# Optimization experiments

Hardware: AMD Instinct MI355X
Metric: run time of the kernel (lower is better)

Reference implementation:

```python
import jax, jax.numpy as jnp
import numpy as np
from jax import lax

A = -0.75  # torch bicubic cubic-kernel coefficient

def _cubic(t):
    t = jnp.abs(t)
    return jnp.where(t <= 1.0, ((A + 2.0) * t - (A + 3.0)) * t * t + 1.0,
                     jnp.where(t < 2.0, A * (((t - 5.0) * t + 8.0) * t - 4.0), 0.0))

def _up2_1d(x, axis):
    # torch F.interpolate(scale_factor=2, mode='bicubic', align_corners=False) along one axis
    n = x.shape[axis]
    src = (jnp.arange(2 * n, dtype=jnp.float32) + 0.5) / 2.0 - 0.5
    i0 = jnp.floor(src).astype(jnp.int32)
    taps = i0[:, None] + jnp.arange(-1, 3)          # [2n,4]
    w = _cubic(src[:, None] - taps.astype(jnp.float32))
    g = jnp.take(x, jnp.clip(taps, 0, n - 1), axis=axis)  # clamp = border replicate
    wshape = [1] * g.ndim
    wshape[axis] = 2 * n
    wshape[axis + 1] = 4
    return jnp.sum(g * w.reshape(wshape), axis=axis + 1)

def bicubic_x2(x):
    return _up2_1d(_up2_1d(x, 2), 3)

def conv2d(x, w, b, stride=1, pad=0):
    y = lax.conv_general_dilated(x, w, (stride, stride), [(pad, pad), (pad, pad)],
                                 dimension_numbers=('NCHW', 'OIHW', 'NCHW'))
    return y + b[None, :, None, None]

def lrelu(x):
    return jax.nn.leaky_relu(x, 0.2)

def resblock(x, w1, b1, w2, b2):
    return x + conv2d(jax.nn.relu(conv2d(x, w1, b1, pad=1)), w2, b2, pad=1)

def feat_head(x, cw, cb, rw1, rb1, rw2, rb2):
    # Conv2d(3,32,5,p=2) -> LReLU -> ResBlock(32) -> LReLU
    return lrelu(resblock(lrelu(conv2d(x, cw, cb, pad=2)), rw1, rb1, rw2, rb2))

def setup_inputs() -> dict:
    key = jax.random.key(0)
    ks = jax.random.split(key, 16)
    def w(k, shape):
        fan = shape[1] * shape[2] * shape[3]
        return jax.random.normal(k, shape, jnp.float32) / np.sqrt(fan)
    def bvec(k, n):
        return jax.random.normal(k, (n,), jnp.float32) * 0.01
    return {
        'x':     jax.random.normal(ks[0], (1, 64, 320, 320), jnp.float32),
        'query': jax.random.normal(ks[1], (1, 3, 160, 160), jnp.float32),
        'ref':   jax.random.normal(ks[2], (1, 3, 320, 320), jnp.float32),
        'conv1_w': w(ks[3], (32, 3, 5, 5)),   'conv1_b': bvec(ks[4], 32),
        'r1_w1':   w(ks[5], (32, 32, 3, 3)),  'r1_b1':   bvec(ks[6], 32),
        'r1_w2':   w(ks[7], (32, 32, 3, 3)),  'r1_b2':   bvec(ks[8], 32),
        'p1_w':    w(ks[9], (32, 64, 5, 5)),  'p1_b':    bvec(ks[10], 32),
        'pr_w1':   w(ks[11], (32, 32, 3, 3)), 'pr_b1':   bvec(ks[12], 32),
        'pr_w2':   w(ks[13], (32, 32, 3, 3)), 'pr_b2':   bvec(ks[14], 32),
        'p2_w':    w(ks[15], (3, 32, 1, 1)),  'p2_b':    jnp.zeros((3,), jnp.float32),
    }

def reference(x, query, ref, conv1_w, conv1_b, r1_w1, r1_b1, r1_w2, r1_b2,
              p1_w, p1_b, pr_w1, pr_b1, pr_w2, pr_b2, p2_w, p2_b):
    ks = 2
    qf = feat_head(bicubic_x2(query), conv1_w, conv1_b, r1_w1, r1_b1, r1_w2, r1_b2)
    rf = feat_head(ref, conv1_w, conv1_b, r1_w1, r1_b1, r1_w2, r1_b2)
    feat = jnp.concatenate([rf, qf], axis=1)  # [b,64,h,w]
    hid = lrelu(resblock(lrelu(conv2d(feat, p1_w, p1_b, pad=2)), pr_w1, pr_b1, pr_w2, pr_b2))
    affine = conv2d(hid, p2_w, p2_b, pad=0) + 1.0   # [b,3,h,w]
    affine = jnp.clip(affine, -3.0, 3.0)
    xp = jnp.pad(x, ((0, 0), (0, 0), (1, 1), (1, 1)), mode='reflect')
    b, c, hp, wp = xp.shape
    h, w = affine.shape[2], affine.shape[3]
    aff = jnp.transpose(affine, (0, 2, 3, 1))       # [b,h,w,3]
    s_x, s_y = aff[..., 0:1], aff[..., 1:2]
    theta = (aff[..., 2:3] - 1.0) * 1.0472          # +/- 60 degrees
    # kernel grid (ks=2): meshgrid('ij') of [-0.5, 0.5], flattened
    pn_x = jnp.array([-0.5, -0.5, 0.5, 0.5], dtype=xp.dtype)
    pn_y = jnp.array([-0.5, 0.5, -0.5, 0.5], dtype=xp.dtype)
    px = pn_x * s_x                                  # [b,h,w,4]
    py = pn_y * s_y
    ct, st = jnp.cos(theta), jnp.sin(theta)
    # [px,py] @ [[c, s],[-s, c]]
    rx = px * ct - py * st
    ry = px * st + py * ct
    off = (ks - 1) // 2 + 0.5                        # 0.5
    p0x = jnp.arange(1, h + 1, dtype=xp.dtype)[None, :, None, None]
    p0y = jnp.arange(1, w + 1, dtype=xp.dtype)[None, None, :, None]
    p_x = rx + off + p0x
    p_y = ry + off + p0y
    lt_x = jnp.floor(lax.stop_gradient(p_x))
    lt_y = jnp.floor(lax.stop_gradient(p_y))
    rb_x, rb_y = lt_x + 1.0, lt_y + 1.0
    lt_xc = jnp.clip(lt_x, 0, hp - 1); lt_yc = jnp.clip(lt_y, 0, wp - 1)
    rb_xc = jnp.clip(rb_x, 0, hp - 1); rb_yc = jnp.clip(rb_y, 0, wp - 1)
    p_x = jnp.clip(p_x, 0, hp - 1); p_y = jnp.clip(p_y, 0, wp - 1)
    g_lt = (1.0 + lt_xc - p_x) * (1.0 + lt_yc - p_y)
    g_rb = (1.0 - (rb_xc - p_x)) * (1.0 - (rb_yc - p_y))
    g_lb = (1.0 + lt_xc - p_x) * (1.0 - (rb_yc - p_y))
    g_rt = (1.0 - (rb_xc - p_x)) * (1.0 + lt_yc - p_y)
    x_flat = xp.reshape(b, c, hp * wp)
    def gather(qx, qy):
        idx = qx.astype(jnp.int32) * wp + qy.astype(jnp.int32)  # [b,h,w,4]
        return jax.vmap(lambda xf, ix: xf[:, ix])(x_flat, idx)   # [b,c,h,w,4]
    align = (g_lt[:, None] * gather(lt_xc, lt_yc)
             + g_rb[:, None] * gather(rb_xc, rb_yc)
             + g_lb[:, None] * gather(lt_xc, rb_yc)
             + g_rt[:, None] * gather(rb_xc, lt_yc))
    # pixel-shuffle style reshape: N index = ix*ks + iy (from 'ij' meshgrid)
    out = align.reshape(b, c, h, w, ks, ks).transpose(0, 1, 2, 4, 3, 5).reshape(b, c, h * ks, w * ks)
    return out
```

## Files before the change

kernel.cpp:

```cpp
#include <hip/hip_runtime.h>

#define H 320
#define W 320
#define HW (H * W)
#define CH 64

typedef _Float16 f16;
typedef _Float16 f16x8 __attribute__((ext_vector_type(8)));
typedef float f32x16 __attribute__((ext_vector_type(16)));

__device__ __forceinline__ float cubw(float t) {
    t = fabsf(t);
    if (t <= 1.f) return (1.25f * t - 2.25f) * t * t + 1.f;
    if (t < 2.f)  return -0.75f * (((t - 5.f) * t + 8.f) * t - 4.f);
    return 0.f;
}

__global__ __launch_bounds__(256) void bicubic_k(const float* __restrict__ q,
                                                 float* __restrict__ outp) {
    int idx = blockIdx.x * 256 + threadIdx.x;
    if (idx >= 3 * HW) return;
    int c = idx / HW;
    int r = idx - c * HW;
    int oy = r / W, ox = r - (r / W) * W;
    float sy = oy * 0.5f - 0.25f;
    float sx = ox * 0.5f - 0.25f;
    int iy0 = (int)floorf(sy);
    int ix0 = (int)floorf(sx);
    float wy[4], wx[4];
    int tyi[4], txi[4];
#pragma unroll
    for (int a = 0; a < 4; a++) {
        int ty = iy0 - 1 + a;
        wy[a] = cubw(sy - (float)ty);
        tyi[a] = min(max(ty, 0), 159);
        int tx = ix0 - 1 + a;
        wx[a] = cubw(sx - (float)tx);
        txi[a] = min(max(tx, 0), 159);
    }
    const float* ip = q + c * (160 * 160);
    float o = 0.f;
#pragma unroll
    for (int b = 0; b < 4; b++) {
        float s = 0.f;
#pragma unroll
        for (int a = 0; a < 4; a++) s += wy[a] * ip[tyi[a] * 160 + txi[b]];
        o += wx[b] * s;
    }
    outp[idx] = o;
}

__global__ __launch_bounds__(256) void repack_k(const float* __restrict__ w0,
                                                const float* __restrict__ w1,
                                                const float* __restrict__ w2,
                                                const float* __restrict__ w3,
                                                const float* __restrict__ w4,
                                                const float* __restrict__ w5,
                                                f16* __restrict__ dst) {
    int li = blockIdx.x * 256 + threadIdx.x;
    if (li >= 11328) return;
    if (li >= 11008) {
        int rel = li - 11008;
        int kc = rel >> 6, l = rel & 63;
        int oc = l & 31, kh = l >> 5;
#pragma unroll
        for (int i = 0; i < 8; ++i) {
            int k = kc * 16 + kh * 8 + i;
            f16 v = (f16)0.f;
            if (k < 75) {
                int tap = k / 3, ic = k - 3 * tap;
                v = (f16)w5[(oc * 3 + ic) * 25 + tap];
            }
            dst[88064 + rel * 8 + i] = v;
        }
        return;
    }
    const float* src;
    int CIN, KS2, base, rel;
    if (li < 1152)       { src = w0; CIN = 32; KS2 = 9;  base = 0;     rel = li; }
    else if (li < 2304)  { src = w1; CIN = 32; KS2 = 9;  base = 9216;  rel = li - 1152; }
    else if (li < 3456)  { src = w2; CIN = 32; KS2 = 9;  base = 18432; rel = li - 2304; }
    else if (li < 4608)  { src = w3; CIN = 32; KS2 = 9;  base = 27648; rel = li - 3456; }
    else                 { src = w4; CIN = 64; KS2 = 25; base = 36864; rel = li - 4608; }
    int fi = rel >> 6, l = rel & 63;
    int kc = fi / KS2, t = fi - kc * KS2;
    int oc = l & 31, kh = l >> 5;
#pragma unroll
    for (int i = 0; i < 8; ++i) {
        int ic = kc * 16 + kh * 8 + i;
        dst[base + rel * 8 + i] = (f16)src[(oc * CIN + ic) * KS2 + t];
    }
}

__global__ __launch_bounds__(256) void hconv_m(const float* __restrict__ in0,
                                               const float* __restrict__ in1,
                                               const f16* __restrict__ wr5,
                                               const float* __restrict__ bias,
                                               f16* __restrict__ out) {
    __shared__ float tile[3][12][40];
    const int b = blockIdx.x >= 400 ? 1 : 0;
    const int tb = blockIdx.x - b * 400;
    const float* in = b ? in1 : in0;
    f16* o = out + (size_t)b * (32 * HW);
    const int x0 = (tb % 10) * 32, y0 = (tb / 10) * 8;
    const int tid = threadIdx.x;

    for (int idx = tid; idx < 1440; idx += 256) {
        int ic = idx / 480;
        int rem = idx - ic * 480;
        int r = rem / 40, c = rem - r * 40;
        int gy = y0 - 2 + r, gx = x0 - 2 + c;
        float v = 0.f;
        if (gy >= 0 && gy < H && gx >= 0 && gx < W)
            v = in[ic * HW + gy * W + gx];
        tile[ic][r][c] = v;
    }
    __syncthreads();

    const int lane = tid & 63, wv = tid >> 6;
    const int R = lane & 31, hh = lane >> 5;

    f32x16 acc0, acc1;
#pragma unroll
    for (int j = 0; j < 16; ++j) { acc0[j] = 0.f; acc1[j] = 0.f; }

#pragma unroll
    for (int kc = 0; kc < 5; ++kc) {
        f16x8 B = *reinterpret_cast<const f16x8*>(wr5 + (kc * 64 + lane) * 8);
#pragma unroll
        for (int m = 0; m < 2; ++m) {
            f16x8 A;
#pragma unroll
            for (int i = 0; i < 8; ++i) {
                int k = kc * 16 + hh * 8 + i;
                float v = 0.f;
                if (k < 75) {
                    int tap = k / 3, ic = k - 3 * tap;
                    int dy = tap / 5, dx = tap - 5 * dy;
                    v = tile[ic][2 * wv + m + dy][R + dx];
                }
                A[i] = (f16)v;
            }
            if (m == 0) acc0 = __builtin_amdgcn_mfma_f32_32x32x16_f16(A, B, acc0, 0, 0, 0);
            else        acc1 = __builtin_amdgcn_mfma_f32_32x32x16_f16(A, B, acc1, 0, 0, 0);
        }
    }

    const float bv = bias[R];
#pragma unroll
    for (int m = 0; m < 2; ++m) {
        const int gy = y0 + 2 * wv + m;
        f32x16 a = m ? acc1 : acc0;
#pragma unroll
        for (int r = 0; r < 16; ++r) {
            int X = x0 + (r & 3) + 8 * (r >> 2) + 4 * hh;
            float v = a[r] + bv;
            v = (v > 0.f) ? v : 0.2f * v;
            o[(gy * W + X) * 32 + R] = (f16)v;
        }
    }
}

template <int KS, int CIN, int ACT, bool RES>
__global__ __launch_bounds__(256) void mconv_k(const f16* __restrict__ in,
                                               const f16* __restrict__ wrep,
                                               const float* __restrict__ bias,
                                               const f16* __restrict__ res,
                                               f16* __restrict__ out,
                                               int OUTC, int inStr, int resStr,
                                               int outStr, int oc0Base, int oc0Step) {
    constexpr int PAD = KS / 2;
    constexpr int TY = 8 + 2 * PAD;
    constexpr int TX = 32 + 2 * PAD;
    constexpr int NPX = TY * TX;
    constexpr int NU = CIN / 4;
    constexpr int UM = NU - 1;
    constexpr int KC = CIN / 16;
    constexpr int KS2 = KS * KS;

    __shared__ uint2 lds2[NPX * NU];

    const int b = blockIdx.x >= 400 ? 1 : 0;
    const int tb = blockIdx.x - b * 400;
    in  += (size_t)b * inStr;
    res += (size_t)b * resStr;
    out += (size_t)b * outStr;
    const int oc0 = oc0Base + b * oc0Step;

    const int tid = threadIdx.x;
    const int bx = tb % 10;
    const int by = tb / 10;
    const int x0 = bx * 32, y0 = by * 8;

    {
        const int cu = tid & UM;
        constexpr int STEP = 256 / NU;
        for (int p = tid / NU; p < NPX; p += STEP) {
            int ly = p / TX, lx = p - ly * TX;
            int gy = y0 - PAD + ly, gx = x0 - PAD + lx;
            uint2 v; v.x = 0u; v.y = 0u;
            if (gy >= 0 && gy < H && gx >= 0 && gx < W)
                v = *reinterpret_cast<const uint2*>(in + (gy * W + gx) * CIN + cu * 4);
            lds2[p * NU + (cu ^ (p & UM))] = v;
        }
    }
    __syncthreads();

    const int lane = tid & 63;
    const int wv = tid >> 6;
    const int R = lane & 31;
    const int hh = lane >> 5;

    f32x16 acc0, acc1;
#pragma unroll
    for (int j = 0; j < 16; ++j) { acc0[j] = 0.f; acc1[j] = 0.f; }

#pragma unroll
    for (int kc = 0; kc < KC; ++kc) {
#pragma unroll
        for (int t = 0; t < KS2; ++t) {
            const int dy = t / KS, dx = t - dy * KS;
            f16x8 B = *reinterpret_cast<const f16x8*>(
                wrep + ((kc * KS2 + t) * 64 + lane) * 8);
            const int u0 = (kc * 2 + hh) * 2;
            {
                int p = (2 * wv + 0 + dy) * TX + R + dx;
                union { uint2 u[2]; f16x8 v; } A;
                A.u[0] = lds2[p * NU + ((u0)     ^ (p & UM))];
                A.u[1] = lds2[p * NU + ((u0 + 1) ^ (p & UM))];
                acc0 = __builtin_amdgcn_mfma_f32_32x32x16_f16(A.v, B, acc0, 0, 0, 0);
            }
            {
                int p = (2 * wv + 1 + dy) * TX + R + dx;
                union { uint2 u[2]; f16x8 v; } A;
                A.u[0] = lds2[p * NU + ((u0)     ^ (p & UM))];
                A.u[1] = lds2[p * NU + ((u0 + 1) ^ (p & UM))];
                acc1 = __builtin_amdgcn_mfma_f32_32x32x16_f16(A.v, B, acc1, 0, 0, 0);
            }
        }
    }

    const float bv = bias[R];
#pragma unroll
    for (int m = 0; m < 2; ++m) {
        const int gy = y0 + 2 * wv + m;
        f32x16 a = m ? acc1 : acc0;
#pragma unroll
        for (int r = 0; r < 16; ++r) {
            int X = x0 + (r & 3) + 8 * (r >> 2) + 4 * hh;
            int pix = gy * W + X;
            float v = a[r] + bv;
            if constexpr (RES) v += (float)res[pix * 32 + R];
            if constexpr (ACT == 0) v = fmaxf(v, 0.f);
            else                    v = (v > 0.f) ? v : 0.2f * v;
            out[pix * OUTC + oc0 + R] = (f16)v;
        }
    }
}

__global__ __launch_bounds__(256) void affine_k(const f16* __restrict__ hid,
                                                const float* __restrict__ w,
                                                const float* __restrict__ b,
                                                float* __restrict__ outp) {
    int p = blockIdx.x * 256 + threadIdx.x;
    if (p >= HW) return;
    const f16x8* hv = reinterpret_cast<const f16x8*>(hid + p * 32);
    float a0 = 0.f, a1 = 0.f, a2 = 0.f;
#pragma unroll
    for (int cc = 0; cc < 4; ++cc) {
        f16x8 hb = hv[cc];
#pragma unroll
        for (int j = 0; j < 8; ++j) {
            float hval = (float)hb[j];
            int c = cc * 8 + j;
            a0 += hval * w[c];
            a1 += hval * w[32 + c];
            a2 += hval * w[64 + c];
        }
    }
    a0 = fminf(fmaxf(a0 + b[0] + 1.f, -3.f), 3.f);
    a1 = fminf(fmaxf(a1 + b[1] + 1.f, -3.f), 3.f);
    a2 = fminf(fmaxf(a2 + b[2] + 1.f, -3.f), 3.f);
    outp[p] = a0;
    outp[HW + p] = a1;
    outp[2 * HW + p] = a2;
}

__device__ __forceinline__ int reflmap(int q) {
    int s = q - 1;
    if (s < 0) s = -s;
    else if (s > 319) s = 638 - s;
    return s;
}

__global__ __launch_bounds__(256) void sample_k(const float* __restrict__ x,
                                                const float* __restrict__ aff,
                                                float* __restrict__ outp) {
    __shared__ float tile[16 * 6 * 80];
    int bid = blockIdx.x;
    bid = (bid & 7) * 800 + (bid >> 3);
    const int cg = bid / 1600;
    const int tb = bid - cg * 1600;
    const int h = tb / 5;
    const int q = tb - 5 * h;
    const int tid = threadIdx.x;
    const int ow = q * 128 + (tid & 127);
    const int oh = 2 * h + (tid >> 7);

    const int w = ow >> 1;
    const int ky = ow & 1, kx = oh & 1;
    const int p = h * W + w;
    float s_x = aff[p];
    float s_y = aff[HW + p];
    float th = (aff[2 * HW + p] - 1.f) * 1.0472f;
    float pnx = kx ? 0.5f : -0.5f;
    float pny = ky ? 0.5f : -0.5f;
    float px = pnx * s_x, py = pny * s_y;
    float st, ct;
    __sincosf(th, &st, &ct);
    float rx = px * ct - py * st;
    float ry = px * st + py * ct;
    float p_x = rx + 0.5f + (float)(h + 1);
    float p_y = ry + 0.5f + (float)(w + 1);
    float ltx = floorf(p_x), lty = floorf(p_y);
    float rbx = ltx + 1.f, rby = lty + 1.f;
    float ltxc = fminf(fmaxf(ltx, 0.f), 321.f);
    float ltyc = fminf(fmaxf(lty, 0.f), 321.f);
    float rbxc = fminf(fmaxf(rbx, 0.f), 321.f);
    float rbyc = fminf(fmaxf(rby, 0.f), 321.f);
    p_x = fminf(fmaxf(p_x, 0.f), 321.f);
    p_y = fminf(fmaxf(p_y, 0.f), 321.f);
    float gx0 = 1.f + ltxc - p_x;
    float gx1 = 1.f - (rbxc - p_x);
    float gy0 = 1.f + ltyc - p_y;
    float gy1 = 1.f - (rbyc - p_y);
    float g_lt = gx0 * gy0, g_rb = gx1 * gy1, g_lb = gx0 * gy1, g_rt = gx1 * gy0;
    int ix0 = reflmap((int)ltxc), ix1 = reflmap((int)rbxc);
    int iy0 = reflmap((int)ltyc), iy1 = reflmap((int)rbyc);

    const int rowbase = h - 2;
    const int colbase = q * 64 - 4;
    const int o00 = (ix0 - rowbase) * 80 + (iy0 - colbase);
    const int o01 = (ix0 - rowbase) * 80 + (iy1 - colbase);
    const int o10 = (ix1 - rowbase) * 80 + (iy0 - colbase);
    const int o11 = (ix1 - rowbase) * 80 + (iy1 - colbase);
    const int obase = oh * 640 + ow;
    const int ch0 = cg * 16;

    for (int idx = tid; idx < 1728; idx += 256) {
        int ch = idx / 108;
        int rem = idx - ch * 108;
        int row = rem / 18;
        int g = rem - row * 18;
        int rv = rowbase + row;
        int cv = colbase + 4 * g;
        float4 v = make_float4(0.f, 0.f, 0.f, 0.f);
        if (rv >= 0 && rv < H && cv >= 0 && cv < W)
            v = *reinterpret_cast<const float4*>(x + (size_t)(ch0 + ch) * HW + rv * W + cv);
        *reinterpret_cast<float4*>(&tile[ch * 480 + row * 80 + 4 * g]) = v;
    }
    __syncthreads();

#pragma unroll
    for (int c = 0; c < 16; ++c) {
        const float* t = tile + c * 480;
        float v = g_lt * t[o00] + g_rb * t[o11] + g_lb * t[o01] + g_rt * t[o10];
        __builtin_nontemporal_store(v, outp + (size_t)(ch0 + c) * (640 * 640) + obase);
    }
}

extern "C" void kernel_launch(void* const* d_in, const int* in_sizes, int n_in,
                              void* d_out, int out_size, void* d_ws, size_t ws_size,
                              hipStream_t stream) {
    const float* x       = (const float*)d_in[0];
    const float* query   = (const float*)d_in[1];
    const float* ref     = (const float*)d_in[2];
    const float* conv1_w = (const float*)d_in[3];
    const float* conv1_b = (const float*)d_in[4];
    const float* r1_w1   = (const float*)d_in[5];
    const float* r1_b1   = (const float*)d_in[6];
    const float* r1_w2   = (const float*)d_in[7];
    const float* r1_b2   = (const float*)d_in[8];
    const float* p1_w    = (const float*)d_in[9];
    const float* p1_b    = (const float*)d_in[10];
    const float* pr_w1   = (const float*)d_in[11];
    const float* pr_b1   = (const float*)d_in[12];
    const float* pr_w2   = (const float*)d_in[13];
    const float* pr_b2   = (const float*)d_in[14];
    const float* p2_w    = (const float*)d_in[15];
    const float* p2_b    = (const float*)d_in[16];

    float* outp = (float*)d_out;
    float* ws = (float*)d_ws;

    float* qup    = ws;
    float* affine = ws + 3 * HW;
    f16* feat = (f16*)outp;
    f16* Bt   = (f16*)(outp + 32 * HW);
    f16* Ct   = (f16*)(outp + 64 * HW);
    f16* Dt   = (f16*)(outp + 96 * HW);
    f16* wrep = (f16*)(outp + 112 * HW);

    repack_k<<<45, 256, 0, stream>>>(r1_w1, r1_w2, pr_w1, pr_w2, p1_w, conv1_w, wrep);
    bicubic_k<<<1200, 256, 0, stream>>>(query, qup);

    hconv_m<<<800, 256, 0, stream>>>(qup, ref, wrep + 88064, conv1_b, Bt);
    mconv_k<3, 32, 0, false><<<800, 256, 0, stream>>>(Bt, wrep,        r1_b1, nullptr, Ct,
                                                      32, 32 * HW, 0, 32 * HW, 0, 0);
    mconv_k<3, 32, 1, true ><<<800, 256, 0, stream>>>(Ct, wrep + 9216, r1_b2, Bt, feat,
                                                      64, 32 * HW, 32 * HW, 0, 32, -32);

    mconv_k<5, 64, 1, false><<<400, 256, 0, stream>>>(feat, wrep + 36864, p1_b, nullptr, Bt,
                                                      32, 0, 0, 0, 0, 0);
    mconv_k<3, 32, 0, false><<<400, 256, 0, stream>>>(Bt, wrep + 18432, pr_b1, nullptr, Ct,
                                                      32, 0, 0, 0, 0, 0);
    mconv_k<3, 32, 1, true ><<<400, 256, 0, stream>>>(Ct, wrep + 27648, pr_b2, Bt, Dt,
                                                      32, 0, 0, 0, 0, 0);

    affine_k<<<400, 256, 0, stream>>>(Dt, p2_w, p2_b, affine);

    sample_k<<<6400, 256, 0, stream>>>(x, affine, outp);
}
```

Measured before the change: 273.4 us.

## Fuse bicubic upsample into first conv and shrink conv/sample tiles

The standalone bicubic kernel is removed and the upsampling is computed inline in hconv_m's tile load, which removes one launch and a round trip of the upsampled image through global memory. The cost is recomputing each bicubic sample for every halo overlap. The mconv kernel gains a rows-per-wave template parameter, so the 3x3 convolutions use 4-row tiles and twice as many blocks. sample_k now handles 8 channels per block instead of 16, doubling the grid. The smaller tiles are meant to raise occupancy and parallelism, at the price of more halo reloads.

```diff
diff --git a/kernel.cpp b/kernel.cpp
--- a/kernel.cpp
+++ b/kernel.cpp
@@ -16,38 +16,27 @@
     return 0.f;
 }
 
-__global__ __launch_bounds__(256) void bicubic_k(const float* __restrict__ q,
-                                                 float* __restrict__ outp) {
-    int idx = blockIdx.x * 256 + threadIdx.x;
-    if (idx >= 3 * HW) return;
-    int c = idx / HW;
-    int r = idx - c * HW;
-    int oy = r / W, ox = r - (r / W) * W;
-    float sy = oy * 0.5f - 0.25f;
-    float sx = ox * 0.5f - 0.25f;
-    int iy0 = (int)floorf(sy);
-    int ix0 = (int)floorf(sx);
-    float wy[4], wx[4];
-    int tyi[4], txi[4];
-#pragma unroll
-    for (int a = 0; a < 4; a++) {
-        int ty = iy0 - 1 + a;
-        wy[a] = cubw(sy - (float)ty);
-        tyi[a] = min(max(ty, 0), 159);
-        int tx = ix0 - 1 + a;
-        wx[a] = cubw(sx - (float)tx);
-        txi[a] = min(max(tx, 0), 159);
-    }
-    const float* ip = q + c * (160 * 160);
+__device__ __forceinline__ float bicub(const float* __restrict__ qc, int gy, int gx) {
+    float sy = gy * 0.5f - 0.25f;
+    float sx = gx * 0.5f - 0.25f;
+    int iy0 = (int)floorf(sy), ix0 = (int)floorf(sx);
     float o = 0.f;
 #pragma unroll
     for (int b = 0; b < 4; b++) {
+        int tx = ix0 - 1 + b;
+        float wxv = cubw(sx - (float)tx);
+        int txc = min(max(tx, 0), 159);
         float s = 0.f;
 #pragma unroll
-        for (int a = 0; a < 4; a++) s += wy[a] * ip[tyi[a] * 160 + txi[b]];
-        o += wx[b] * s;
-    }
-    outp[idx] = o;
+        for (int a = 0; a < 4; a++) {
+            int ty = iy0 - 1 + a;
+            float wyv = cubw(sy - (float)ty);
+            int tyc = min(max(ty, 0), 159);
+            s += wyv * qc[tyc * 160 + txc];
+        }
+        o += wxv * s;
+    }
+    return o;
 }
 
 __global__ __launch_bounds__(256) void repack_k(const float* __restrict__ w0,
@@ -92,15 +81,14 @@
     }
 }
 
-__global__ __launch_bounds__(256) void hconv_m(const float* __restrict__ in0,
-                                               const float* __restrict__ in1,
+__global__ __launch_bounds__(256) void hconv_m(const float* __restrict__ query,
+                                               const float* __restrict__ ref,
                                                const f16* __restrict__ wr5,
                                                const float* __restrict__ bias,
                                                f16* __restrict__ out) {
     __shared__ float tile[3][12][40];
     const int b = blockIdx.x >= 400 ? 1 : 0;
     const int tb = blockIdx.x - b * 400;
-    const float* in = b ? in1 : in0;
     f16* o = out + (size_t)b * (32 * HW);
     const int x0 = (tb % 10) * 32, y0 = (tb / 10) * 8;
     const int tid = threadIdx.x;
@@ -112,7 +100,8 @@
         int gy = y0 - 2 + r, gx = x0 - 2 + c;
         float v = 0.f;
         if (gy >= 0 && gy < H && gx >= 0 && gx < W)
-            v = in[ic * HW + gy * W + gx];
+            v = b ? ref[ic * HW + gy * W + gx]
+                  : bicub(query + ic * 25600, gy, gx);
         tile[ic][r][c] = v;
     }
     __syncthreads();
@@ -161,7 +150,7 @@
     }
 }
 
-template <int KS, int CIN, int ACT, bool RES>
+template <int KS, int CIN, int ACT, bool RES, int R2W>
 __global__ __launch_bounds__(256) void mconv_k(const f16* __restrict__ in,
                                                const f16* __restrict__ wrep,
                                                const float* __restrict__ bias,
@@ -170,18 +159,20 @@
                                                int OUTC, int inStr, int resStr,
                                                int outStr, int oc0Base, int oc0Step) {
     constexpr int PAD = KS / 2;
-    constexpr int TY = 8 + 2 * PAD;
+    constexpr int TROWS = 4 * R2W;
+    constexpr int TY = TROWS + 2 * PAD;
     constexpr int TX = 32 + 2 * PAD;
     constexpr int NPX = TY * TX;
     constexpr int NU = CIN / 4;
     constexpr int UM = NU - 1;
     constexpr int KC = CIN / 16;
     constexpr int KS2 = KS * KS;
+    constexpr int BPB = 800 / R2W;
 
     __shared__ uint2 lds2[NPX * NU];
 
-    const int b = blockIdx.x >= 400 ? 1 : 0;
-    const int tb = blockIdx.x - b * 400;
+    const int b = blockIdx.x >= BPB ? 1 : 0;
+    const int tb = blockIdx.x - b * BPB;
     in  += (size_t)b * inStr;
     res += (size_t)b * resStr;
     out += (size_t)b * outStr;
@@ -190,7 +181,7 @@
     const int tid = threadIdx.x;
     const int bx = tb % 10;
     const int by = tb / 10;
-    const int x0 = bx * 32, y0 = by * 8;
+    const int x0 = bx * 32, y0 = by * TROWS;
 
     {
         const int cu = tid & UM;
@@ -224,14 +215,14 @@
                 wrep + ((kc * KS2 + t) * 64 + lane) * 8);
             const int u0 = (kc * 2 + hh) * 2;
             {
-                int p = (2 * wv + 0 + dy) * TX + R + dx;
+                int p = (R2W * wv + 0 + dy) * TX + R + dx;
                 union { uint2 u[2]; f16x8 v; } A;
                 A.u[0] = lds2[p * NU + ((u0)     ^ (p & UM))];
                 A.u[1] = lds2[p * NU + ((u0 + 1) ^ (p & UM))];
                 acc0 = __builtin_amdgcn_mfma_f32_32x32x16_f16(A.v, B, acc0, 0, 0, 0);
             }
-            {
-                int p = (2 * wv + 1 + dy) * TX + R + dx;
+            if constexpr (R2W == 2) {
+                int p = (R2W * wv + 1 + dy) * TX + R + dx;
                 union { uint2 u[2]; f16x8 v; } A;
                 A.u[0] = lds2[p * NU + ((u0)     ^ (p & UM))];
                 A.u[1] = lds2[p * NU + ((u0 + 1) ^ (p & UM))];
@@ -242,8 +233,8 @@
 
     const float bv = bias[R];
 #pragma unroll
-    for (int m = 0; m < 2; ++m) {
-        const int gy = y0 + 2 * wv + m;
+    for (int m = 0; m < R2W; ++m) {
+        const int gy = y0 + R2W * wv + m;
         f32x16 a = m ? acc1 : acc0;
 #pragma unroll
         for (int r = 0; r < 16; ++r) {
@@ -296,9 +287,9 @@
 __global__ __launch_bounds__(256) void sample_k(const float* __restrict__ x,
                                                 const float* __restrict__ aff,
                                                 float* __restrict__ outp) {
-    __shared__ float tile[16 * 6 * 80];
+    __shared__ float tile[8 * 6 * 80];
     int bid = blockIdx.x;
-    bid = (bid & 7) * 800 + (bid >> 3);
+    bid = (bid & 7) * 1600 + (bid >> 3);
     const int cg = bid / 1600;
     const int tb = bid - cg * 1600;
     const int h = tb / 5;
@@ -345,9 +336,9 @@
     const int o10 = (ix1 - rowbase) * 80 + (iy0 - colbase);
     const int o11 = (ix1 - rowbase) * 80 + (iy1 - colbase);
     const int obase = oh * 640 + ow;
-    const int ch0 = cg * 16;
-
-    for (int idx = tid; idx < 1728; idx += 256) {
+    const int ch0 = cg * 8;
+
+    for (int idx = tid; idx < 864; idx += 256) {
         int ch = idx / 108;
         int rem = idx - ch * 108;
         int row = rem / 18;
@@ -362,7 +353,7 @@
     __syncthreads();
 
 #pragma unroll
-    for (int c = 0; c < 16; ++c) {
+    for (int c = 0; c < 8; ++c) {
         const float* t = tile + c * 480;
         float v = g_lt * t[o00] + g_rb * t[o11] + g_lb * t[o01] + g_rt * t[o10];
         __builtin_nontemporal_store(v, outp + (size_t)(ch0 + c) * (640 * 640) + obase);
@@ -393,8 +384,7 @@
     float* outp = (float*)d_out;
     float* ws = (float*)d_ws;
 
-    float* qup    = ws;
-    float* affine = ws + 3 * HW;
+    float* affine = ws;
     f16* feat = (f16*)outp;
     f16* Bt   = (f16*)(outp + 32 * HW);
     f16* Ct   = (f16*)(outp + 64 * HW);
@@ -402,22 +392,21 @@
     f16* wrep = (f16*)(outp + 112 * HW);
 
     repack_k<<<45, 256, 0, stream>>>(r1_w1, r1_w2, pr_w1, pr_w2, p1_w, conv1_w, wrep);
-    bicubic_k<<<1200, 256, 0, stream>>>(query, qup);
-
-    hconv_m<<<800, 256, 0, stream>>>(qup, ref, wrep + 88064, conv1_b, Bt);
-    mconv_k<3, 32, 0, false><<<800, 256, 0, stream>>>(Bt, wrep,        r1_b1, nullptr, Ct,
-                                                      32, 32 * HW, 0, 32 * HW, 0, 0);
-    mconv_k<3, 32, 1, true ><<<800, 256, 0, stream>>>(Ct, wrep + 9216, r1_b2, Bt, feat,
-                                                      64, 32 * HW, 32 * HW, 0, 32, -32);
-
-    mconv_k<5, 64, 1, false><<<400, 256, 0, stream>>>(feat, wrep + 36864, p1_b, nullptr, Bt,
-                                                      32, 0, 0, 0, 0, 0);
-    mconv_k<3, 32, 0, false><<<400, 256, 0, stream>>>(Bt, wrep + 18432, pr_b1, nullptr, Ct,
-                                                      32, 0, 0, 0, 0, 0);
-    mconv_k<3, 32, 1, true ><<<400, 256, 0, stream>>>(Ct, wrep + 27648, pr_b2, Bt, Dt,
-                                                      32, 0, 0, 0, 0, 0);
+
+    hconv_m<<<800, 256, 0, stream>>>(query, ref, wrep + 88064, conv1_b, Bt);
+    mconv_k<3, 32, 0, false, 1><<<1600, 256, 0, stream>>>(Bt, wrep,        r1_b1, nullptr, Ct,
+                                                          32, 32 * HW, 0, 32 * HW, 0, 0);
+    mconv_k<3, 32, 1, true , 1><<<1600, 256, 0, stream>>>(Ct, wrep + 9216, r1_b2, Bt, feat,
+                                                          64, 32 * HW, 32 * HW, 0, 32, -32);
+
+    mconv_k<5, 64, 1, false, 2><<<400, 256, 0, stream>>>(feat, wrep + 36864, p1_b, nullptr, Bt,
+                                                         32, 0, 0, 0, 0, 0);
+    mconv_k<3, 32, 0, false, 1><<<800, 256, 0, stream>>>(Bt, wrep + 18432, pr_b1, nullptr, Ct,
+                                                         32, 0, 0, 0, 0, 0);
+    mconv_k<3, 32, 1, true , 1><<<800, 256, 0, stream>>>(Ct, wrep + 27648, pr_b2, Bt, Dt,
+                                                         32, 0, 0, 0, 0, 0);
 
     affine_k<<<400, 256, 0, stream>>>(Dt, p2_w, p2_b, affine);
 
-    sample_k<<<6400, 256, 0, stream>>>(x, affine, outp);
-}
+    sample_k<<<12800, 256, 0, stream>>>(x, affine, outp);
+}
```

Result: faster. 267.4 us (-2.2%).
